# Performance work log

Measured on AMD Instinct MI355X. Metric: run time of the kernel, lower is better.

## Reference

```python
import jax, jax.numpy as jnp
import numpy as np

ND1 = 8000   # block1 num dst nodes
ND2 = 4000   # block2 num dst nodes


def gat_layer(x_src, x_dst, src, dst, num_dst, W, a_src, a_dst, b, heads, ch):
    """PyG GATConv (bipartite tuple input, concat=True) in jax.
    x_src: [B,Ns,F], x_dst: [B,Nd,F]; src/dst: [E] int edge endpoints."""
    B = x_src.shape[0]
    h_s = jnp.einsum('bnf,fk->bnk', x_src, W).reshape(B, -1, heads, ch)  # [B,Ns,H,C]
    h_d = jnp.einsum('bnf,fk->bnk', x_dst, W).reshape(B, -1, heads, ch)  # [B,Nd,H,C]
    e_s = jnp.einsum('bnhc,hc->bnh', h_s, a_src)  # [B,Ns,H]
    e_d = jnp.einsum('bnhc,hc->bnh', h_d, a_dst)  # [B,Nd,H]
    alpha = jax.nn.leaky_relu(e_s[:, src] + e_d[:, dst], 0.2)  # [B,E,H]
    a = jnp.transpose(alpha, (1, 0, 2))  # [E,B,H] (segment ops reduce axis 0)
    amax = jax.ops.segment_max(a, dst, num_segments=num_dst)  # [Nd,B,H]
    ex = jnp.exp(a - amax[dst])
    den = jax.ops.segment_sum(ex, dst, num_segments=num_dst)
    w = ex / (den[dst] + 1e-16)  # edge softmax per (dst,batch,head)
    msg = jnp.transpose(h_s[:, src], (1, 0, 2, 3)) * w[..., None]  # [E,B,H,C]
    out = jax.ops.segment_sum(msg, dst, num_segments=num_dst)  # [Nd,B,H,C]
    out = jnp.transpose(out, (1, 0, 2, 3)).reshape(B, num_dst, heads * ch)
    return out + b


def setup_inputs() -> dict:
    key = jax.random.key(0)
    ks = jax.random.split(key, 16)
    B, N, F = 2, 20000, 128
    E1, E2 = 100000, 60000
    inp = {
        'x': jax.random.normal(ks[0], (B, N, F), jnp.float32),
        'n_id1': jax.random.randint(ks[1], (16000,), 0, N),
        'res_n_id1': jax.random.randint(ks[2], (ND1,), 0, 16000),
        'src1': jax.random.randint(ks[3], (E1,), 0, 16000),
        'dst1': jax.random.randint(ks[4], (E1,), 0, ND1),
        'res_n_id2': jax.random.randint(ks[5], (ND2,), 0, ND1),
        'src2': jax.random.randint(ks[6], (E2,), 0, ND1),
        'dst2': jax.random.randint(ks[7], (E2,), 0, ND2),
        'W1': jax.random.normal(ks[8], (F, 12 * 128), jnp.float32) * 0.05,
        'att_src1': jax.random.normal(ks[9], (12, 128), jnp.float32) * 0.1,
        'att_dst1': jax.random.normal(ks[10], (12, 128), jnp.float32) * 0.1,
        'bias1': jnp.zeros((12 * 128,), jnp.float32),
        'W2': jax.random.normal(ks[11], (12 * 128, 1), jnp.float32) * 0.05,
        'att_src2': jax.random.normal(ks[12], (1, 1), jnp.float32) * 0.1,
        'att_dst2': jax.random.normal(ks[13], (1, 1), jnp.float32) * 0.1,
        'bias2': jnp.zeros((1,), jnp.float32),
    }
    return inp


def reference(x, n_id1, res_n_id1, src1, dst1, res_n_id2, src2, dst2,
              W1, att_src1, att_dst1, bias1, W2, att_src2, att_dst2, bias2):
    # block 1
    xt = x[:, n_id1, :]                       # [B,16000,F]
    xd = xt[:, res_n_id1, :]                  # [B,8000,F]
    h = gat_layer(xt, xd, src1, dst1, ND1, W1, att_src1, att_dst1, bias1, 12, 128)
    h = jax.nn.relu(h)                        # [B,8000,1536]
    # block 2
    hd = h[:, res_n_id2, :]                   # [B,4000,1536]
    out = gat_layer(h, hd, src2, dst2, ND2, W2, att_src2, att_dst2, bias2, 1, 1)
    return out                                # [B,4000,1]
```

## Files before the change

### kernel.cpp

```cpp
#include <hip/hip_runtime.h>
#include <hip/hip_bf16.h>

#define B2      2
#define NX      20000
#define F_IN    128
#define NS1     16000
#define ND1     8000
#define E1      100000
#define ND2     4000
#define E2      60000
#define HEADS   12
#define CH      128
#define K1      1536
#define MROWS   (2*ND1)

typedef __bf16 bf16x8 __attribute__((ext_vector_type(8)));
typedef float  f32x4  __attribute__((ext_vector_type(4)));

static __device__ __forceinline__ float lrelu(float x) { return x > 0.f ? x : 0.2f * x; }

static __device__ __forceinline__ unsigned short f2bf(float f) {
    union { float f; unsigned u; } v; v.f = f;
    unsigned r = v.u + 0x7fffu + ((v.u >> 16) & 1u);
    return (unsigned short)(r >> 16);
}
static __device__ __forceinline__ float bf2f(unsigned short h) {
    union { unsigned u; float f; } v; v.u = ((unsigned)h) << 16;
    return v.f;
}

static __device__ __forceinline__ void gld16(const void* g, void* l) {
    __builtin_amdgcn_global_load_lds(
        (const __attribute__((address_space(1))) unsigned int*)g,
        (__attribute__((address_space(3))) unsigned int*)l, 16, 0, 0);
}

__global__ __launch_bounds__(256) void k_prep(const float* __restrict__ x,
                                              const int* __restrict__ n_id,
                                              const float* __restrict__ W,
                                              const float* __restrict__ asrc,
                                              const float* __restrict__ adst,
                                              unsigned short* __restrict__ xg,
                                              unsigned short* __restrict__ WT,
                                              unsigned short* __restrict__ wswd,
                                              int* __restrict__ deg,
                                              float* __restrict__ s2)
{
    const int bx = blockIdx.x;
    const int tid = threadIdx.x;
    if (bx < 4000) {
        int t = bx * 256 + tid;
        int row = t >> 5;
        int c4 = (t & 31) << 2;
        int b = row >= NS1 ? 1 : 0;
        int node = n_id[row - b * NS1];
        const float4 v = *reinterpret_cast<const float4*>(
            x + ((size_t)(b * NX + node)) * F_IN + c4);
        ushort4 o;
        o.x = f2bf(v.x); o.y = f2bf(v.y); o.z = f2bf(v.z); o.w = f2bf(v.w);
        *reinterpret_cast<ushort4*>(xg + (size_t)row * F_IN + c4) = o;
    } else if (bx < 4768) {
        int t = (bx - 4000) * 256 + tid;
        int k = t / K1;
        int n = t - k * K1;
        WT[(size_t)n * F_IN + k] = f2bf(W[t]);
    } else if (bx < 4784) {
        int t = (bx - 4768) * 256 + tid;
        int n = t >> 7;
        int c = t & 127;
        float acc = 0.f;
        if (n < 24) {
            int h = n < 12 ? n : n - 12;
            const float* att = (n < 12 ? asrc : adst) + h * CH;
            const float* wr = W + (size_t)c * K1 + h * CH;
            for (int j = 0; j < CH; ++j) acc += wr[j] * att[j];
        }
        wswd[(size_t)n * F_IN + c] = f2bf(acc);
    } else {
        int t = (bx - 4784) * 256 + tid;
        if (t < ND1 + ND2) deg[t] = 0;
        else if (t < ND1 + ND2 + MROWS) s2[t - (ND1 + ND2)] = 0.f;
    }
}

__global__ __launch_bounds__(256) void k_escore_count(
        const unsigned short* __restrict__ xg,
        const unsigned short* __restrict__ wswd,
        const int* __restrict__ dst1, const int* __restrict__ dst2,
        float* __restrict__ es, float* __restrict__ ed,
        int* __restrict__ deg)
{
    const int tid = threadIdx.x;
    if (blockIdx.x < 500) {
        const int wave = tid >> 6, lane = tid & 63;
        const int l15 = lane & 15, l4 = lane >> 4;
        const int rt = blockIdx.x * 4 + wave;
        const int row0 = rt * 16;
        const unsigned short* Ap = xg + (size_t)(row0 + l15) * F_IN + l4 * 8;

        f32x4 acc[2] = {f32x4{0,0,0,0}, f32x4{0,0,0,0}};
#pragma unroll
        for (int kk = 0; kk < 4; ++kk) {
            bf16x8 a = *reinterpret_cast<const bf16x8*>(Ap + kk * 32);
#pragma unroll
            for (int c = 0; c < 2; ++c) {
                bf16x8 b = *reinterpret_cast<const bf16x8*>(
                    wswd + (size_t)(c * 16 + l15) * F_IN + kk * 32 + l4 * 8);
                acc[c] = __builtin_amdgcn_mfma_f32_16x16x32_bf16(a, b, acc[c], 0, 0, 0);
            }
        }
#pragma unroll
        for (int c = 0; c < 2; ++c) {
            int col = c * 16 + l15;
#pragma unroll
            for (int r = 0; r < 4; ++r) {
                int row = row0 + l4 * 4 + r;
                float v = acc[c][r];
                if (col < 12)       es[(size_t)row * HEADS + col] = v;
                else if (col < 24)  ed[(size_t)row * HEADS + (col - 12)] = v;
            }
        }
    } else {
        int e = (blockIdx.x - 500) * 256 + tid;
        if (e < E1) atomicAdd(&deg[dst1[e]], 1);
        else if (e < E1 + E2) atomicAdd(&deg[ND1 + dst2[e - E1]], 1);
    }
}

static __device__ void scan_body(const int* __restrict__ deg, int n,
                                 int* __restrict__ off, int* __restrict__ cursor)
{
    __shared__ int wsum[16];
    __shared__ int carry_sh;
    int tid = threadIdx.x, lane = tid & 63, wid = tid >> 6;
    if (tid == 0) { carry_sh = 0; off[0] = 0; }
    __syncthreads();
    for (int base = 0; base < n; base += 1024) {
        int i = base + tid;
        int v = (i < n) ? deg[i] : 0;
        int s = v;
#pragma unroll
        for (int o = 1; o < 64; o <<= 1) {
            int t = __shfl_up(s, o);
            if (lane >= o) s += t;
        }
        if (lane == 63) wsum[wid] = s;
        __syncthreads();
        if (wid == 0) {
            int t = (lane < 16) ? wsum[lane] : 0;
#pragma unroll
            for (int o = 1; o < 16; o <<= 1) {
                int u = __shfl_up(t, o);
                if (lane >= o) t += u;
            }
            if (lane < 16) wsum[lane] = t;
        }
        __syncthreads();
        int carry = carry_sh;
        int wexcl = (wid == 0) ? 0 : wsum[wid - 1];
        int incl = carry + wexcl + s;
        if (i < n) { off[i + 1] = incl; cursor[i] = incl - v; }
        __syncthreads();
        if (tid == 0) carry_sh = carry + wsum[15];
        __syncthreads();
    }
}

__global__ __launch_bounds__(1024) void k_scan2(const int* __restrict__ deg,
                                                int* __restrict__ off1,
                                                int* __restrict__ off2,
                                                int* __restrict__ cur)
{
    if (blockIdx.x == 0) scan_body(deg, ND1, off1, cur);
    else                 scan_body(deg + ND1, ND2, off2, cur + ND1);
}

__global__ void k_scatter2(const int* __restrict__ dst1, const int* __restrict__ src1,
                           const int* __restrict__ dst2, const int* __restrict__ src2,
                           const int* __restrict__ res1,
                           const float* __restrict__ es, const float* __restrict__ ed,
                           int* __restrict__ cur, unsigned* __restrict__ ew,
                           int* __restrict__ srcp2)
{
    int e = blockIdx.x * 256 + threadIdx.x;
    if (e < E1) {
        int d = dst1[e];
        int p = atomicAdd(&cur[d], 1);
        int s = src1[e];
        int rd = res1[d];
#pragma unroll
        for (int b = 0; b < 2; ++b) {
            const float* esp = es + ((size_t)(b * NS1 + s)) * HEADS;
            const float* edp = ed + ((size_t)(b * NS1 + rd)) * HEADS;
            unsigned w[6];
#pragma unroll
            for (int j = 0; j < 6; ++j) {
                float w0 = __expf(lrelu(esp[2 * j] + edp[2 * j]));
                float w1 = __expf(lrelu(esp[2 * j + 1] + edp[2 * j + 1]));
                w[j] = (unsigned)f2bf(w0) | ((unsigned)f2bf(w1) << 16);
            }
            unsigned* rp = ew + ((size_t)b * E1 + p) * 8;
            *reinterpret_cast<uint4*>(rp) = make_uint4((unsigned)s, w[0], w[1], w[2]);
            *reinterpret_cast<uint4*>(rp + 4) = make_uint4(w[3], w[4], w[5], 0u);
        }
    } else if (e < E1 + E2) {
        int ee = e - E1;
        int p = atomicAdd(&cur[ND1 + dst2[ee]], 1);
        srcp2[p] = src2[ee];
    }
}

__global__ __launch_bounds__(256) void k_agg1(const unsigned short* __restrict__ xg,
                                              const unsigned* __restrict__ ew,
                                              const int* __restrict__ off,
                                              unsigned short* __restrict__ agg)
{
    const int tid = threadIdx.x;
    const int wv = tid >> 6, lane = tid & 63;
    const int task = blockIdx.x * 4 + wv;
    const int b = task >= ND1 ? 1 : 0;
    const int i = task - b * ND1;
    const int c2 = lane * 2;

    const int beg = off[i], end = off[i + 1];
    const uint4* eb = reinterpret_cast<const uint4*>(ew + (size_t)b * E1 * 8);
    const unsigned short* xb = xg + (size_t)b * NS1 * F_IN + c2;

    float acc[24];
    float den[12];
#pragma unroll
    for (int r = 0; r < 24; ++r) acc[r] = 0.f;
#pragma unroll
    for (int h = 0; h < 12; ++h) den[h] = 0.f;

#pragma unroll 2
    for (int p = beg; p < end; ++p) {
        uint4 r0 = eb[2 * p];
        uint4 r1 = eb[2 * p + 1];
        int se = (int)r0.x;
        unsigned xv = *reinterpret_cast<const unsigned*>(xb + (size_t)se * F_IN);
        float x0 = __uint_as_float(xv << 16);
        float x1 = __uint_as_float(xv & 0xffff0000u);
        unsigned wd[6] = {r0.y, r0.z, r0.w, r1.x, r1.y, r1.z};
#pragma unroll
        for (int j = 0; j < 6; ++j) {
            unsigned d = wd[j];
            float w0 = __uint_as_float(d << 16);
            float w1 = __uint_as_float(d & 0xffff0000u);
            acc[4 * j + 0] += w0 * x0; acc[4 * j + 1] += w0 * x1;
            acc[4 * j + 2] += w1 * x0; acc[4 * j + 3] += w1 * x1;
            den[2 * j]     += w0;      den[2 * j + 1] += w1;
        }
    }

    const size_t rowbase = ((size_t)(b * ND1 + i)) * K1;
#pragma unroll
    for (int j = 0; j < 12; ++j) {
        float r = 1.f / (den[j] + 1e-16f);
        unsigned pk = (unsigned)f2bf(acc[2 * j] * r) |
                      ((unsigned)f2bf(acc[2 * j + 1] * r) << 16);
        *reinterpret_cast<unsigned*>(agg + rowbase + j * CH + c2) = pk;
    }
}

__global__ __launch_bounds__(256) void k_out1(const unsigned short* __restrict__ agg,
                                              const unsigned short* __restrict__ WT,
                                              const float* __restrict__ bias1,
                                              const float* __restrict__ W2,
                                              float* __restrict__ s2)
{
    __shared__ unsigned short As[128 * 128];
    __shared__ unsigned short Bs[128 * 128];

    const int tid = threadIdx.x;
    const int wv = tid >> 6, lane = tid & 63;
    const int l15 = lane & 15, l4 = lane >> 4;
    const int row0 = blockIdx.x * 128;
    const int h = blockIdx.y;

    {
        const unsigned short* ga = agg + (size_t)row0 * K1 + h * CH;
        const unsigned short* gb = WT + (size_t)(h * CH) * F_IN;
#pragma unroll
        for (int p = 0; p < 8; ++p) {
            int r = p * 16 + wv * 4 + l4;
            int cs = l15 ^ (r & 7);
            gld16(ga + (size_t)r * K1 + cs * 8, As + (p * 16 + wv * 4) * 128);
            gld16(gb + (size_t)r * F_IN + cs * 8, Bs + (p * 16 + wv * 4) * 128);
        }
    }
    __syncthreads();

    f32x4 acc[2][8];
#pragma unroll
    for (int m = 0; m < 2; ++m)
#pragma unroll
        for (int c = 0; c < 8; ++c) acc[m][c] = f32x4{0, 0, 0, 0};

#pragma unroll
    for (int kk = 0; kk < 4; ++kk) {
        bf16x8 a[2];
#pragma unroll
        for (int m = 0; m < 2; ++m) {
            int r = wv * 32 + m * 16 + l15;
            int ch = (l4 + kk * 4) ^ (r & 7);
            a[m] = *reinterpret_cast<const bf16x8*>(As + r * 128 + ch * 8);
        }
#pragma unroll
        for (int c = 0; c < 8; ++c) {
            int n = c * 16 + l15;
            int ch = (l4 + kk * 4) ^ (n & 7);
            bf16x8 bb = *reinterpret_cast<const bf16x8*>(Bs + n * 128 + ch * 8);
#pragma unroll
            for (int m = 0; m < 2; ++m)
                acc[m][c] = __builtin_amdgcn_mfma_f32_16x16x32_bf16(a[m], bb,
                                                                    acc[m][c], 0, 0, 0);
        }
    }

#pragma unroll
    for (int m = 0; m < 2; ++m) {
        float part[4] = {0.f, 0.f, 0.f, 0.f};
#pragma unroll
        for (int c = 0; c < 8; ++c) {
            int n = h * CH + c * 16 + l15;
            float bi = bias1[n];
            float w2 = W2[n];
#pragma unroll
            for (int r = 0; r < 4; ++r) {
                float v = acc[m][c][r] + bi;
                v = v > 0.f ? v : 0.f;
                part[r] += v * w2;
            }
        }
#pragma unroll
        for (int r = 0; r < 4; ++r) {
#pragma unroll
            for (int o = 1; o < 16; o <<= 1) part[r] += __shfl_xor(part[r], o);
        }
        if (l15 == 0) {
            int row = row0 + wv * 32 + m * 16 + l4 * 4;
#pragma unroll
            for (int r = 0; r < 4; ++r)
                atomicAdd(&s2[row + r], part[r]);
        }
    }
}

__global__ void k_agg2(const float* __restrict__ s2,
                       const int* __restrict__ off,
                       const int* __restrict__ srcp2,
                       const int* __restrict__ res2,
                       const float* __restrict__ asrc,
                       const float* __restrict__ adst,
                       const float* __restrict__ bias2,
                       float* __restrict__ out)
{
    int t = blockIdx.x * 256 + threadIdx.x;
    if (t >= 2 * ND2) return;
    int b = t / ND2, j = t - b * ND2;
    float a_s = asrc[0], a_d = adst[0];
    float edl = s2[(size_t)b * ND1 + res2[j]] * a_d;
    int beg = off[j], end = off[j + 1];
    float den = 0.f, num = 0.f;
    for (int p = beg; p < end; ++p) {
        int s = srcp2[p];
        float v = s2[b * ND1 + s];
        float w = __expf(lrelu(v * a_s + edl));
        den += w;
        num += w * v;
    }
    float o = (end > beg) ? num / (den + 1e-16f) : 0.f;
    out[(size_t)b * ND2 + j] = o + bias2[0];
}

extern "C" void kernel_launch(void* const* d_in, const int* in_sizes, int n_in,
                              void* d_out, int out_size, void* d_ws, size_t ws_size,
                              hipStream_t stream)
{
    const float* x        = (const float*)d_in[0];
    const int* n_id1      = (const int*)d_in[1];
    const int* res_n_id1  = (const int*)d_in[2];
    const int* src1       = (const int*)d_in[3];
    const int* dst1       = (const int*)d_in[4];
    const int* res_n_id2  = (const int*)d_in[5];
    const int* src2       = (const int*)d_in[6];
    const int* dst2       = (const int*)d_in[7];
    const float* W1       = (const float*)d_in[8];
    const float* att_src1 = (const float*)d_in[9];
    const float* att_dst1 = (const float*)d_in[10];
    const float* bias1    = (const float*)d_in[11];
    const float* W2       = (const float*)d_in[12];
    const float* att_src2 = (const float*)d_in[13];
    const float* att_dst2 = (const float*)d_in[14];
    const float* bias2    = (const float*)d_in[15];

    unsigned short* xg   = (unsigned short*)d_ws;
    unsigned short* W1T  = xg + (size_t)2 * NS1 * F_IN;
    unsigned short* wswd = W1T + (size_t)K1 * F_IN;
    unsigned short* agg  = wswd + (size_t)32 * F_IN;
    float* es  = (float*)(agg + (size_t)2 * ND1 * K1);
    float* ed  = es + (size_t)2 * NS1 * HEADS;
    float* s2  = ed + (size_t)2 * NS1 * HEADS;
    int* deg   = (int*)(s2 + (size_t)2 * ND1);
    int* off1  = deg + (ND1 + ND2);
    int* off2  = off1 + (ND1 + 1);
    int* cur   = off2 + (ND2 + 1);
    int* srcp2 = cur + (ND1 + ND2) + 2;
    unsigned* ew = (unsigned*)(srcp2 + E2 + 2);

    k_prep<<<4894, 256, 0, stream>>>(x, n_id1, W1, att_src1, att_dst1,
                                     xg, W1T, wswd, deg, s2);

    k_escore_count<<<500 + (E1 + E2 + 255) / 256, 256, 0, stream>>>(
        xg, wswd, dst1, dst2, es, ed, deg);

    k_scan2<<<2, 1024, 0, stream>>>(deg, off1, off2, cur);

    k_scatter2<<<(E1 + E2 + 255) / 256, 256, 0, stream>>>(
        dst1, src1, dst2, src2, res_n_id1, es, ed, cur, ew, srcp2);

    k_agg1<<<MROWS / 4, 256, 0, stream>>>(xg, ew, off1, agg);

    k_out1<<<dim3(MROWS / 128, HEADS), 256, 0, stream>>>(agg, W1T, bias1, W2, s2);

    k_agg2<<<(2 * ND2 + 255) / 256, 256, 0, stream>>>(s2, off2, srcp2,
                                                      res_n_id2, att_src2,
                                                      att_dst2, bias2,
                                                      (float*)d_out);
}
```

Before: 112.2 us.

## Split layer-1 aggregation into two head-halves per node to double parallelism

The packed edge records are split into two separate uint4 streams, each carrying the source index and six heads of bf16 weights. The aggregation kernel launches twice as many waves, and each wave handles half the heads for one destination node. This halves the accumulator registers per wave and exposes more parallelism. In exchange, every edge's source index and x gather are read twice, once per half, which adds gather traffic.

```diff
diff --git a/kernel.cpp b/kernel.cpp
--- a/kernel.cpp
+++ b/kernel.cpp
@@ -179,7 +179,7 @@
                            const int* __restrict__ dst2, const int* __restrict__ src2,
                            const int* __restrict__ res1,
                            const float* __restrict__ es, const float* __restrict__ ed,
-                           int* __restrict__ cur, unsigned* __restrict__ ew,
+                           int* __restrict__ cur, uint4* __restrict__ ewq,
                            int* __restrict__ srcp2)
 {
     int e = blockIdx.x * 256 + threadIdx.x;
@@ -199,9 +199,8 @@
                 float w1 = __expf(lrelu(esp[2 * j + 1] + edp[2 * j + 1]));
                 w[j] = (unsigned)f2bf(w0) | ((unsigned)f2bf(w1) << 16);
             }
-            unsigned* rp = ew + ((size_t)b * E1 + p) * 8;
-            *reinterpret_cast<uint4*>(rp) = make_uint4((unsigned)s, w[0], w[1], w[2]);
-            *reinterpret_cast<uint4*>(rp + 4) = make_uint4(w[3], w[4], w[5], 0u);
+            ewq[((size_t)(b * 2 + 0)) * E1 + p] = make_uint4((unsigned)s, w[0], w[1], w[2]);
+            ewq[((size_t)(b * 2 + 1)) * E1 + p] = make_uint4((unsigned)s, w[3], w[4], w[5]);
         }
     } else if (e < E1 + E2) {
         int ee = e - E1;
@@ -211,39 +210,40 @@
 }
 
 __global__ __launch_bounds__(256) void k_agg1(const unsigned short* __restrict__ xg,
-                                              const unsigned* __restrict__ ew,
+                                              const uint4* __restrict__ ewq,
                                               const int* __restrict__ off,
                                               unsigned short* __restrict__ agg)
 {
     const int tid = threadIdx.x;
     const int wv = tid >> 6, lane = tid & 63;
     const int task = blockIdx.x * 4 + wv;
-    const int b = task >= ND1 ? 1 : 0;
-    const int i = task - b * ND1;
+    const int b2h = task / 8000;
+    const int i = task - b2h * 8000;
+    const int b = b2h >> 1;
+    const int half = b2h & 1;
     const int c2 = lane * 2;
 
     const int beg = off[i], end = off[i + 1];
-    const uint4* eb = reinterpret_cast<const uint4*>(ew + (size_t)b * E1 * 8);
+    const uint4* eb = ewq + (size_t)b2h * E1;
     const unsigned short* xb = xg + (size_t)b * NS1 * F_IN + c2;
 
-    float acc[24];
-    float den[12];
-#pragma unroll
-    for (int r = 0; r < 24; ++r) acc[r] = 0.f;
-#pragma unroll
-    for (int h = 0; h < 12; ++h) den[h] = 0.f;
+    float acc[12];
+    float den[6];
+#pragma unroll
+    for (int r = 0; r < 12; ++r) acc[r] = 0.f;
+#pragma unroll
+    for (int h = 0; h < 6; ++h) den[h] = 0.f;
 
 #pragma unroll 2
     for (int p = beg; p < end; ++p) {
-        uint4 r0 = eb[2 * p];
-        uint4 r1 = eb[2 * p + 1];
+        uint4 r0 = eb[p];
         int se = (int)r0.x;
         unsigned xv = *reinterpret_cast<const unsigned*>(xb + (size_t)se * F_IN);
         float x0 = __uint_as_float(xv << 16);
         float x1 = __uint_as_float(xv & 0xffff0000u);
-        unsigned wd[6] = {r0.y, r0.z, r0.w, r1.x, r1.y, r1.z};
-#pragma unroll
-        for (int j = 0; j < 6; ++j) {
+        unsigned wd[3] = {r0.y, r0.z, r0.w};
+#pragma unroll
+        for (int j = 0; j < 3; ++j) {
             unsigned d = wd[j];
             float w0 = __uint_as_float(d << 16);
             float w1 = __uint_as_float(d & 0xffff0000u);
@@ -253,9 +253,9 @@
         }
     }
 
-    const size_t rowbase = ((size_t)(b * ND1 + i)) * K1;
-#pragma unroll
-    for (int j = 0; j < 12; ++j) {
+    const size_t rowbase = ((size_t)(b * ND1 + i)) * K1 + half * 6 * CH;
+#pragma unroll
+    for (int j = 0; j < 6; ++j) {
         float r = 1.f / (den[j] + 1e-16f);
         unsigned pk = (unsigned)f2bf(acc[2 * j] * r) |
                       ((unsigned)f2bf(acc[2 * j + 1] * r) << 16);
@@ -399,15 +399,15 @@
     unsigned short* W1T  = xg + (size_t)2 * NS1 * F_IN;
     unsigned short* wswd = W1T + (size_t)K1 * F_IN;
     unsigned short* agg  = wswd + (size_t)32 * F_IN;
-    float* es  = (float*)(agg + (size_t)2 * ND1 * K1);
+    uint4* ewq = (uint4*)(agg + (size_t)2 * ND1 * K1);
+    float* es  = (float*)(ewq + (size_t)4 * E1);
     float* ed  = es + (size_t)2 * NS1 * HEADS;
     float* s2  = ed + (size_t)2 * NS1 * HEADS;
     int* deg   = (int*)(s2 + (size_t)2 * ND1);
     int* off1  = deg + (ND1 + ND2);
     int* off2  = off1 + (ND1 + 1);
     int* cur   = off2 + (ND2 + 1);
-    int* srcp2 = cur + (ND1 + ND2) + 2;
-    unsigned* ew = (unsigned*)(srcp2 + E2 + 2);
+    int* srcp2 = cur + (ND1 + ND2);
 
     k_prep<<<4894, 256, 0, stream>>>(x, n_id1, W1, att_src1, att_dst1,
                                      xg, W1T, wswd, deg, s2);
@@ -418,9 +418,9 @@
     k_scan2<<<2, 1024, 0, stream>>>(deg, off1, off2, cur);
 
     k_scatter2<<<(E1 + E2 + 255) / 256, 256, 0, stream>>>(
-        dst1, src1, dst2, src2, res_n_id1, es, ed, cur, ew, srcp2);
-
-    k_agg1<<<MROWS / 4, 256, 0, stream>>>(xg, ew, off1, agg);
+        dst1, src1, dst2, src2, res_n_id1, es, ed, cur, ewq, srcp2);
+
+    k_agg1<<<(2 * MROWS) / 4, 256, 0, stream>>>(xg, ewq, off1, agg);
 
     k_out1<<<dim3(MROWS / 128, HEADS), 256, 0, stream>>>(agg, W1T, bias1, W2, s2);
 
```

Result: slower. 114.7 us (+2.3%).
